# Performance work log

Measured on AMD Instinct MI355X. Metric: run time of the kernel, lower is better.

The kernel has to match this reference:

```python
import jax, jax.numpy as jnp
import numpy as np

BS, SEQ, DIM, DIM_MLP, E = 2, 2048, 1024, 4096, 8
STD = 0.02  # nn.init.normal_(weight, std=0.02)


def setup_inputs() -> dict:
    key = jax.random.key(0)
    k_x, k_idx, k_w1, k_w2 = jax.random.split(key, 4)
    x = jax.random.normal(k_x, (BS, SEQ, DIM), dtype=jnp.float32)
    expert_idx = jax.random.randint(k_idx, (BS, SEQ), 0, E, dtype=jnp.int32)
    W1 = jax.random.normal(k_w1, (E, DIM, DIM_MLP), dtype=jnp.float32) * STD
    b1 = jnp.zeros((E, DIM_MLP), dtype=jnp.float32)
    W2 = jax.random.normal(k_w2, (E, DIM_MLP, DIM), dtype=jnp.float32) * STD
    b2 = jnp.zeros((E, DIM), dtype=jnp.float32)
    return {"x": x, "expert_idx": expert_idx, "W1": W1, "b1": b1, "W2": W2, "b2": b2}


def reference(x, expert_idx, W1, b1, W2, b2):
    # Compute ALL experts on all tokens (faithful to the torch module).
    # h: [bs, seq, E, dim_mlp]
    h = jnp.einsum("bsd,edm->bsem", x, W1) + b1
    h = jax.nn.gelu(h, approximate=False)  # torch nn.GELU default = exact erf
    # feat: [bs, seq, E, dim]  (== torch.cat along feature dim, reshaped)
    feat = jnp.einsum("bsem,emd->bsed", h, W2) + b2
    # Per-token gather of the assigned expert's output (top-1 select).
    idx = expert_idx.astype(jnp.int32)[:, :, None, None]  # [bs, seq, 1, 1]
    out = jnp.take_along_axis(feat, idx, axis=2)[:, :, 0, :]  # [bs, seq, dim]
    return out
```

## Files before the change

### kernel.cpp

```cpp
#include <hip/hip_runtime.h>
#include <hip/hip_bf16.h>
#include <math.h>

#define TOK   4096
#define DIM   1024
#define DMLP  4096
#define NE    8
#define BM    128
#define BN    128
#define BN2   64
#define BK    64
#define PADMAX (TOK + NE * BM)
#define NTILES (PADMAX / BM)

typedef __attribute__((ext_vector_type(8))) short  short8;
typedef __attribute__((ext_vector_type(4))) float  float4v;
typedef __attribute__((ext_vector_type(4))) unsigned short ushort4v;

#define ASYNC16(gp, lp) __builtin_amdgcn_global_load_lds( \
    (const __attribute__((address_space(1))) unsigned int*)(gp), \
    (__attribute__((address_space(3))) unsigned int*)(lp), 16, 0, 0)

#define FRAG_OFF(R, C) (((((R) << 3) + ((C) ^ ((R) & 7)))) << 3)

static __device__ __forceinline__ unsigned short f2bf(float f) {
  unsigned u = __float_as_uint(f);
  u += 0x7fffu + ((u >> 16) & 1u);
  return (unsigned short)(u >> 16);
}

__global__ void group_kernel(const int* __restrict__ eidx,
                             int* __restrict__ perm,
                             int* __restrict__ tile_e) {
  __shared__ int cnt[NE], off[NE], len[NE], cur[NE];
  const int tid = threadIdx.x;
  if (tid < NE) cnt[tid] = 0;
  __syncthreads();
  for (int i = tid; i < TOK; i += 256) atomicAdd(&cnt[eidx[i]], 1);
  __syncthreads();
  if (tid == 0) {
    int o = 0;
    for (int e = 0; e < NE; e++) {
      off[e] = o;
      len[e] = ((cnt[e] + BM - 1) / BM) * BM;
      cur[e] = o;
      o += len[e];
    }
  }
  __syncthreads();
  for (int s = tid; s < PADMAX; s += 256) perm[s] = -1;
  __syncthreads();
  for (int i = tid; i < TOK; i += 256) {
    const int e = eidx[i];
    const int p = atomicAdd(&cur[e], 1);
    perm[p] = i;
  }
  __syncthreads();
  for (int t = tid; t < NTILES; t += 256) {
    const int row = t * BM;
    int te = -1;
    for (int e = 0; e < NE; e++)
      if (row >= off[e] && row < off[e] + len[e]) te = e;
    tile_e[t] = te;
  }
}

__global__ __launch_bounds__(256)
void convtrans_kernel(const float* __restrict__ W, unsigned short* __restrict__ WT,
                      int K, int N) {
  __shared__ unsigned short T[64][66];
  const int e  = blockIdx.z;
  const int k0 = blockIdx.y * 64, n0 = blockIdx.x * 64;
  const float* Win = W + (size_t)e * K * N;
  unsigned short* Wout = WT + (size_t)e * K * N;
  const int tid = threadIdx.x;
  const int nl  = tid & 63;
  const int kb  = (tid >> 6) * 16;
#pragma unroll
  for (int r = 0; r < 16; r++) {
    const int kl = kb + r;
    T[nl][kl] = f2bf(Win[(size_t)(k0 + kl) * N + n0 + nl]);
  }
  __syncthreads();
  const int kc = (tid & 31) * 2;
  const int nb = tid >> 5;
#pragma unroll
  for (int r = 0; r < 8; r++) {
    const int nl2 = nb + r * 8;
    const unsigned v = *(const unsigned*)&T[nl2][kc];
    *(unsigned*)&Wout[(size_t)(n0 + nl2) * K + k0 + kc] = v;
  }
}

__global__ __launch_bounds__(256)
void xgather_kernel(const float* __restrict__ x, const int* __restrict__ perm,
                    unsigned short* __restrict__ xg) {
  const int slot = blockIdx.x;
  const int t    = perm[slot];
  const int tid  = threadIdx.x;
  ushort4v o = (ushort4v){0, 0, 0, 0};
  if (t >= 0) {
    const float4v v = *(const float4v*)(x + (size_t)t * DIM + tid * 4);
#pragma unroll
    for (int q = 0; q < 4; q++) o[q] = f2bf(v[q]);
  }
  *(ushort4v*)(xg + (size_t)slot * DIM + tid * 4) = o;
}

__global__ __launch_bounds__(256)
void gemm1_kernel(const unsigned short* __restrict__ xg,
                  const unsigned short* __restrict__ W1T,
                  const float* __restrict__ b1, const int* __restrict__ tile_e,
                  unsigned short* __restrict__ h) {
  const int te = tile_e[blockIdx.x];
  if (te < 0) return;
  const unsigned short* Asrc = xg + (size_t)blockIdx.x * BM * DIM;
  const unsigned short* Bsrc = W1T + (size_t)te * DIM * DMLP + (size_t)(blockIdx.y * BN) * DIM;
  const int tid = threadIdx.x;

  __shared__ __align__(16) unsigned short As[BM * BK];
  __shared__ __align__(16) unsigned short Bs[BN * BK];

  const unsigned short* ag[4];
  const unsigned short* bg[4];
  int lo[4];
#pragma unroll
  for (int t = 0; t < 4; t++) {
    const int p = t * 256 + tid;
    const int r = p >> 3;
    const int c = (p & 7) ^ (r & 7);
    ag[t] = Asrc + (size_t)r * DIM + c * 8;
    bg[t] = Bsrc + (size_t)r * DIM + c * 8;
    lo[t] = p * 8;
  }

  const int wid = tid >> 6, lane = tid & 63;
  const int wm = (wid >> 1) * 64, wn = (wid & 1) * 64;
  const int l15 = lane & 15, quad = lane >> 4;

  float4v acc[4][4];
#pragma unroll
  for (int i = 0; i < 4; i++)
#pragma unroll
    for (int j = 0; j < 4; j++) acc[i][j] = (float4v){0.f, 0.f, 0.f, 0.f};

  for (int k0 = 0; k0 < DIM; k0 += BK) {
#pragma unroll
    for (int t = 0; t < 4; t++) ASYNC16(ag[t] + k0, &As[lo[t]]);
#pragma unroll
    for (int t = 0; t < 4; t++) ASYNC16(bg[t] + k0, &Bs[lo[t]]);
    __syncthreads();

#pragma unroll
    for (int hh = 0; hh < 2; hh++) {
      short8 a[4], b[4];
      const int C = hh * 4 + quad;
#pragma unroll
      for (int i = 0; i < 4; i++) a[i] = *(const short8*)&As[FRAG_OFF(wm + i * 16 + l15, C)];
#pragma unroll
      for (int j = 0; j < 4; j++) b[j] = *(const short8*)&Bs[FRAG_OFF(wn + j * 16 + l15, C)];
#pragma unroll
      for (int i = 0; i < 4; i++)
#pragma unroll
        for (int j = 0; j < 4; j++)
          acc[i][j] = __builtin_amdgcn_mfma_f32_16x16x32_bf16(a[i], b[j], acc[i][j], 0, 0, 0);
    }
    __syncthreads();
  }

#pragma unroll
  for (int i = 0; i < 4; i++) {
#pragma unroll
    for (int j = 0; j < 4; j++) {
      const int col = blockIdx.y * BN + wn + j * 16 + l15;
      const float bias = b1[te * DMLP + col];
#pragma unroll
      for (int r = 0; r < 4; r++) {
        const int row = wm + i * 16 + quad * 4 + r;
        float v = acc[i][j][r] + bias;
        v = 0.5f * v * (1.0f + erff(v * 0.7071067811865475f));
        h[(size_t)(blockIdx.x * BM + row) * DMLP + col] = f2bf(v);
      }
    }
  }
}

__global__ __launch_bounds__(256)
void gemm2_kernel(const unsigned short* __restrict__ h,
                  const unsigned short* __restrict__ W2T,
                  const float* __restrict__ b2, const int* __restrict__ perm,
                  const int* __restrict__ tile_e, float* __restrict__ out) {
  const int te = tile_e[blockIdx.x];
  if (te < 0) return;
  const unsigned short* Asrc = h + (size_t)blockIdx.x * BM * DMLP;
  const unsigned short* Bsrc = W2T + (size_t)te * DMLP * DIM + (size_t)(blockIdx.y * BN2) * DMLP;
  const int tid = threadIdx.x;

  __shared__ __align__(16) unsigned short As[BM * BK];
  __shared__ __align__(16) unsigned short Bs[BN2 * BK];

  const unsigned short* ag[4];
  const unsigned short* bg[2];
  int alo[4], blo[2];
#pragma unroll
  for (int t = 0; t < 4; t++) {
    const int p = t * 256 + tid;
    const int r = p >> 3;
    const int c = (p & 7) ^ (r & 7);
    ag[t] = Asrc + (size_t)r * DMLP + c * 8;
    alo[t] = p * 8;
  }
#pragma unroll
  for (int t = 0; t < 2; t++) {
    const int p = t * 256 + tid;
    const int r = p >> 3;
    const int c = (p & 7) ^ (r & 7);
    bg[t] = Bsrc + (size_t)r * DMLP + c * 8;
    blo[t] = p * 8;
  }

  const int wid = tid >> 6, lane = tid & 63;
  const int wm = (wid >> 1) * 64, wn = (wid & 1) * 32;
  const int l15 = lane & 15, quad = lane >> 4;

  float4v acc[4][2];
#pragma unroll
  for (int i = 0; i < 4; i++)
#pragma unroll
    for (int j = 0; j < 2; j++) acc[i][j] = (float4v){0.f, 0.f, 0.f, 0.f};

  for (int k0 = 0; k0 < DMLP; k0 += BK) {
#pragma unroll
    for (int t = 0; t < 4; t++) ASYNC16(ag[t] + k0, &As[alo[t]]);
#pragma unroll
    for (int t = 0; t < 2; t++) ASYNC16(bg[t] + k0, &Bs[blo[t]]);
    __syncthreads();

#pragma unroll
    for (int hh = 0; hh < 2; hh++) {
      short8 a[4], b[2];
      const int C = hh * 4 + quad;
#pragma unroll
      for (int i = 0; i < 4; i++) a[i] = *(const short8*)&As[FRAG_OFF(wm + i * 16 + l15, C)];
#pragma unroll
      for (int j = 0; j < 2; j++) b[j] = *(const short8*)&Bs[FRAG_OFF(wn + j * 16 + l15, C)];
#pragma unroll
      for (int i = 0; i < 4; i++)
#pragma unroll
        for (int j = 0; j < 2; j++)
          acc[i][j] = __builtin_amdgcn_mfma_f32_16x16x32_bf16(a[i], b[j], acc[i][j], 0, 0, 0);
    }
    __syncthreads();
  }

#pragma unroll
  for (int i = 0; i < 4; i++) {
#pragma unroll
    for (int j = 0; j < 2; j++) {
      const int col = blockIdx.y * BN2 + wn + j * 16 + l15;
      const float bias = b2[te * DIM + col];
#pragma unroll
      for (int r = 0; r < 4; r++) {
        const int row  = wm + i * 16 + quad * 4 + r;
        const int slot = blockIdx.x * BM + row;
        const int t    = perm[slot];
        if (t >= 0) out[(size_t)t * DIM + col] = acc[i][j][r] + bias;
      }
    }
  }
}

extern "C" void kernel_launch(void* const* d_in, const int* in_sizes, int n_in,
                              void* d_out, int out_size, void* d_ws, size_t ws_size,
                              hipStream_t stream) {
  const float* x    = (const float*)d_in[0];
  const int*   eidx = (const int*)d_in[1];
  const float* W1   = (const float*)d_in[2];
  const float* b1   = (const float*)d_in[3];
  const float* W2   = (const float*)d_in[4];
  const float* b2   = (const float*)d_in[5];
  float* out = (float*)d_out;

  char* ws = (char*)d_ws;
  int* perm   = (int*)ws;
  int* tile_e = (int*)(ws + PADMAX * sizeof(int));
  unsigned short* xg  = (unsigned short*)(ws + 32768);
  unsigned short* h   = (unsigned short*)(ws + 32768 + 10485760);
  unsigned short* W1T = (unsigned short*)(ws + 32768 + 10485760 + 41943040);
  unsigned short* W2T = (unsigned short*)((char*)W1T + 67108864);

  group_kernel<<<1, 256, 0, stream>>>(eidx, perm, tile_e);
  convtrans_kernel<<<dim3(DMLP / 64, DIM / 64, NE), 256, 0, stream>>>(W1, W1T, DIM, DMLP);
  convtrans_kernel<<<dim3(DIM / 64, DMLP / 64, NE), 256, 0, stream>>>(W2, W2T, DMLP, DIM);
  xgather_kernel<<<PADMAX, 256, 0, stream>>>(x, perm, xg);
  gemm1_kernel<<<dim3(NTILES, DMLP / BN), 256, 0, stream>>>(xg, W1T, b1, tile_e, h);
  gemm2_kernel<<<dim3(NTILES, DIM / BN2), 256, 0, stream>>>(h, W2T, b2, perm, tile_e, out);
}
```

Before: 494.3 us.

## Enlarge GEMM tiles to 256 rows, split-K GEMM2 with atomics, vectorize transpose, fast GELU

The row tile grows to 256 with 512-thread blocks in both GEMMs, and GEMM2 widens its N tile to 128 while splitting K four ways, accumulating into a zeroed output with float atomics. The weight convert-transpose kernel now uses vectorized float4 loads and 16-byte stores. The exact erff GELU is replaced by a polynomial erf approximation using rcp and exp. These changes target redundant weight traffic, occupancy, and epilogue cost, but larger tiles add more padding waste per expert. They also bring atomic contention, an extra zeroing pass, and a small accuracy change in GELU.

Measured after the change: 519.3 us. +5.0%, slower.

```diff
diff --git a/kernel.cpp b/kernel.cpp
--- a/kernel.cpp
+++ b/kernel.cpp
@@ -6,12 +6,14 @@
 #define DIM   1024
 #define DMLP  4096
 #define NE    8
-#define BM    128
+#define BM    256
 #define BN    128
-#define BN2   64
 #define BK    64
+#define NTHR  512
 #define PADMAX (TOK + NE * BM)
 #define NTILES (PADMAX / BM)
+#define KSPLIT 4
+#define KCHUNK (DMLP / KSPLIT)
 
 typedef __attribute__((ext_vector_type(8))) short  short8;
 typedef __attribute__((ext_vector_type(4))) float  float4v;
@@ -27,6 +29,22 @@
   unsigned u = __float_as_uint(f);
   u += 0x7fffu + ((u >> 16) & 1u);
   return (unsigned short)(u >> 16);
+}
+
+static __device__ __forceinline__ float gelu_f(float v) {
+  const float s = v * 0.7071067811865475f;
+  const float a = fabsf(s);
+  const float t = __builtin_amdgcn_rcpf(1.0f + 0.3275911f * a);
+  float p = 1.061405429f;
+  p = p * t - 1.453152027f;
+  p = p * t + 1.421413741f;
+  p = p * t - 0.284496736f;
+  p = p * t + 0.254829592f;
+  p = p * t;
+  const float e = __expf(-s * s);
+  float er = 1.0f - p * e;
+  er = copysignf(er, s);
+  return 0.5f * v * (1.0f + er);
 }
 
 __global__ void group_kernel(const int* __restrict__ eidx,
@@ -66,29 +84,43 @@
 }
 
 __global__ __launch_bounds__(256)
+void zero_out_kernel(float* __restrict__ out) {
+  const int i = blockIdx.x * 256 + threadIdx.x;
+  *(float4v*)(out + (size_t)i * 4) = (float4v){0.f, 0.f, 0.f, 0.f};
+}
+
+__global__ __launch_bounds__(256)
 void convtrans_kernel(const float* __restrict__ W, unsigned short* __restrict__ WT,
                       int K, int N) {
-  __shared__ unsigned short T[64][66];
+  __shared__ unsigned short T[64][68];
   const int e  = blockIdx.z;
   const int k0 = blockIdx.y * 64, n0 = blockIdx.x * 64;
   const float* Win = W + (size_t)e * K * N;
   unsigned short* Wout = WT + (size_t)e * K * N;
   const int tid = threadIdx.x;
-  const int nl  = tid & 63;
-  const int kb  = (tid >> 6) * 16;
-#pragma unroll
-  for (int r = 0; r < 16; r++) {
-    const int kl = kb + r;
-    T[nl][kl] = f2bf(Win[(size_t)(k0 + kl) * N + n0 + nl]);
-  }
-  __syncthreads();
-  const int kc = (tid & 31) * 2;
-  const int nb = tid >> 5;
-#pragma unroll
-  for (int r = 0; r < 8; r++) {
-    const int nl2 = nb + r * 8;
-    const unsigned v = *(const unsigned*)&T[nl2][kc];
-    *(unsigned*)&Wout[(size_t)(n0 + nl2) * K + k0 + kc] = v;
+
+  const int klb = tid >> 4;
+  const int n4  = (tid & 15) * 4;
+#pragma unroll
+  for (int r = 0; r < 4; r++) {
+    const int kl = klb + r * 16;
+    const float4v v = *(const float4v*)(Win + (size_t)(k0 + kl) * N + n0 + n4);
+#pragma unroll
+    for (int q = 0; q < 4; q++) T[n4 + q][kl] = f2bf(v[q]);
+  }
+  __syncthreads();
+
+  const int nlb = tid >> 3;
+  const int kc  = (tid & 7) * 8;
+#pragma unroll
+  for (int w = 0; w < 2; w++) {
+    const int nl = nlb + w * 32;
+    const ushort4v u0 = *(const ushort4v*)&T[nl][kc];
+    const ushort4v u1 = *(const ushort4v*)&T[nl][kc + 4];
+    short8 o;
+#pragma unroll
+    for (int q = 0; q < 4; q++) { o[q] = (short)u0[q]; o[q + 4] = (short)u1[q]; }
+    *(short8*)(Wout + (size_t)(n0 + nl) * K + k0 + kc) = o;
   }
 }
 
@@ -107,7 +139,7 @@
   *(ushort4v*)(xg + (size_t)slot * DIM + tid * 4) = o;
 }
 
-__global__ __launch_bounds__(256)
+__global__ __launch_bounds__(NTHR)
 void gemm1_kernel(const unsigned short* __restrict__ xg,
                   const unsigned short* __restrict__ W1T,
                   const float* __restrict__ b1, const int* __restrict__ tile_e,
@@ -122,16 +154,23 @@
   __shared__ __align__(16) unsigned short Bs[BN * BK];
 
   const unsigned short* ag[4];
-  const unsigned short* bg[4];
-  int lo[4];
+  const unsigned short* bg[2];
+  int alo[4], blo[2];
 #pragma unroll
   for (int t = 0; t < 4; t++) {
-    const int p = t * 256 + tid;
+    const int p = t * NTHR + tid;
     const int r = p >> 3;
     const int c = (p & 7) ^ (r & 7);
     ag[t] = Asrc + (size_t)r * DIM + c * 8;
+    alo[t] = p * 8;
+  }
+#pragma unroll
+  for (int t = 0; t < 2; t++) {
+    const int p = t * NTHR + tid;
+    const int r = p >> 3;
+    const int c = (p & 7) ^ (r & 7);
     bg[t] = Bsrc + (size_t)r * DIM + c * 8;
-    lo[t] = p * 8;
+    blo[t] = p * 8;
   }
 
   const int wid = tid >> 6, lane = tid & 63;
@@ -146,9 +185,9 @@
 
   for (int k0 = 0; k0 < DIM; k0 += BK) {
 #pragma unroll
-    for (int t = 0; t < 4; t++) ASYNC16(ag[t] + k0, &As[lo[t]]);
-#pragma unroll
-    for (int t = 0; t < 4; t++) ASYNC16(bg[t] + k0, &Bs[lo[t]]);
+    for (int t = 0; t < 4; t++) ASYNC16(ag[t] + k0, &As[alo[t]]);
+#pragma unroll
+    for (int t = 0; t < 2; t++) ASYNC16(bg[t] + k0, &Bs[blo[t]]);
     __syncthreads();
 
 #pragma unroll
@@ -177,34 +216,35 @@
 #pragma unroll
       for (int r = 0; r < 4; r++) {
         const int row = wm + i * 16 + quad * 4 + r;
-        float v = acc[i][j][r] + bias;
-        v = 0.5f * v * (1.0f + erff(v * 0.7071067811865475f));
+        const float v = gelu_f(acc[i][j][r] + bias);
         h[(size_t)(blockIdx.x * BM + row) * DMLP + col] = f2bf(v);
       }
     }
   }
 }
 
-__global__ __launch_bounds__(256)
+__global__ __launch_bounds__(NTHR)
 void gemm2_kernel(const unsigned short* __restrict__ h,
                   const unsigned short* __restrict__ W2T,
                   const float* __restrict__ b2, const int* __restrict__ perm,
                   const int* __restrict__ tile_e, float* __restrict__ out) {
   const int te = tile_e[blockIdx.x];
   if (te < 0) return;
-  const unsigned short* Asrc = h + (size_t)blockIdx.x * BM * DMLP;
-  const unsigned short* Bsrc = W2T + (size_t)te * DMLP * DIM + (size_t)(blockIdx.y * BN2) * DMLP;
+  const int kbase = blockIdx.z * KCHUNK;
+  const unsigned short* Asrc = h + (size_t)blockIdx.x * BM * DMLP + kbase;
+  const unsigned short* Bsrc = W2T + (size_t)te * DMLP * DIM
+                             + (size_t)(blockIdx.y * BN) * DMLP + kbase;
   const int tid = threadIdx.x;
 
   __shared__ __align__(16) unsigned short As[BM * BK];
-  __shared__ __align__(16) unsigned short Bs[BN2 * BK];
+  __shared__ __align__(16) unsigned short Bs[BN * BK];
 
   const unsigned short* ag[4];
   const unsigned short* bg[2];
   int alo[4], blo[2];
 #pragma unroll
   for (int t = 0; t < 4; t++) {
-    const int p = t * 256 + tid;
+    const int p = t * NTHR + tid;
     const int r = p >> 3;
     const int c = (p & 7) ^ (r & 7);
     ag[t] = Asrc + (size_t)r * DMLP + c * 8;
@@ -212,7 +252,7 @@
   }
 #pragma unroll
   for (int t = 0; t < 2; t++) {
-    const int p = t * 256 + tid;
+    const int p = t * NTHR + tid;
     const int r = p >> 3;
     const int c = (p & 7) ^ (r & 7);
     bg[t] = Bsrc + (size_t)r * DMLP + c * 8;
@@ -220,16 +260,16 @@
   }
 
   const int wid = tid >> 6, lane = tid & 63;
-  const int wm = (wid >> 1) * 64, wn = (wid & 1) * 32;
+  const int wm = (wid >> 1) * 64, wn = (wid & 1) * 64;
   const int l15 = lane & 15, quad = lane >> 4;
 
-  float4v acc[4][2];
+  float4v acc[4][4];
 #pragma unroll
   for (int i = 0; i < 4; i++)
 #pragma unroll
-    for (int j = 0; j < 2; j++) acc[i][j] = (float4v){0.f, 0.f, 0.f, 0.f};
-
-  for (int k0 = 0; k0 < DMLP; k0 += BK) {
+    for (int j = 0; j < 4; j++) acc[i][j] = (float4v){0.f, 0.f, 0.f, 0.f};
+
+  for (int k0 = 0; k0 < KCHUNK; k0 += BK) {
 #pragma unroll
     for (int t = 0; t < 4; t++) ASYNC16(ag[t] + k0, &As[alo[t]]);
 #pragma unroll
@@ -238,16 +278,16 @@
 
 #pragma unroll
     for (int hh = 0; hh < 2; hh++) {
-      short8 a[4], b[2];
+      short8 a[4], b[4];
       const int C = hh * 4 + quad;
 #pragma unroll
       for (int i = 0; i < 4; i++) a[i] = *(const short8*)&As[FRAG_OFF(wm + i * 16 + l15, C)];
 #pragma unroll
-      for (int j = 0; j < 2; j++) b[j] = *(const short8*)&Bs[FRAG_OFF(wn + j * 16 + l15, C)];
+      for (int j = 0; j < 4; j++) b[j] = *(const short8*)&Bs[FRAG_OFF(wn + j * 16 + l15, C)];
 #pragma unroll
       for (int i = 0; i < 4; i++)
 #pragma unroll
-        for (int j = 0; j < 2; j++)
+        for (int j = 0; j < 4; j++)
           acc[i][j] = __builtin_amdgcn_mfma_f32_16x16x32_bf16(a[i], b[j], acc[i][j], 0, 0, 0);
     }
     __syncthreads();
@@ -256,15 +296,15 @@
 #pragma unroll
   for (int i = 0; i < 4; i++) {
 #pragma unroll
-    for (int j = 0; j < 2; j++) {
-      const int col = blockIdx.y * BN2 + wn + j * 16 + l15;
-      const float bias = b2[te * DIM + col];
+    for (int j = 0; j < 4; j++) {
+      const int col = blockIdx.y * BN + wn + j * 16 + l15;
+      const float bias = (blockIdx.z == 0) ? b2[te * DIM + col] : 0.f;
 #pragma unroll
       for (int r = 0; r < 4; r++) {
         const int row  = wm + i * 16 + quad * 4 + r;
         const int slot = blockIdx.x * BM + row;
         const int t    = perm[slot];
-        if (t >= 0) out[(size_t)t * DIM + col] = acc[i][j][r] + bias;
+        if (t >= 0) atomicAdd(&out[(size_t)t * DIM + col], acc[i][j][r] + bias);
       }
     }
   }
@@ -285,14 +325,15 @@
   int* perm   = (int*)ws;
   int* tile_e = (int*)(ws + PADMAX * sizeof(int));
   unsigned short* xg  = (unsigned short*)(ws + 32768);
-  unsigned short* h   = (unsigned short*)(ws + 32768 + 10485760);
-  unsigned short* W1T = (unsigned short*)(ws + 32768 + 10485760 + 41943040);
-  unsigned short* W2T = (unsigned short*)((char*)W1T + 67108864);
+  unsigned short* h   = (unsigned short*)((char*)xg + (size_t)PADMAX * DIM * 2);
+  unsigned short* W1T = (unsigned short*)((char*)h + (size_t)PADMAX * DMLP * 2);
+  unsigned short* W2T = (unsigned short*)((char*)W1T + (size_t)NE * DIM * DMLP * 2);
 
   group_kernel<<<1, 256, 0, stream>>>(eidx, perm, tile_e);
+  zero_out_kernel<<<(TOK * DIM) / 1024, 256, 0, stream>>>(out);
   convtrans_kernel<<<dim3(DMLP / 64, DIM / 64, NE), 256, 0, stream>>>(W1, W1T, DIM, DMLP);
   convtrans_kernel<<<dim3(DIM / 64, DMLP / 64, NE), 256, 0, stream>>>(W2, W2T, DMLP, DIM);
   xgather_kernel<<<PADMAX, 256, 0, stream>>>(x, perm, xg);
-  gemm1_kernel<<<dim3(NTILES, DMLP / BN), 256, 0, stream>>>(xg, W1T, b1, tile_e, h);
-  gemm2_kernel<<<dim3(NTILES, DIM / BN2), 256, 0, stream>>>(h, W2T, b2, perm, tile_e, out);
-}
+  gemm1_kernel<<<dim3(NTILES, DMLP / BN), NTHR, 0, stream>>>(xg, W1T, b1, tile_e, h);
+  gemm2_kernel<<<dim3(NTILES, DIM / BN, KSPLIT), NTHR, 0, stream>>>(h, W2T, b2, perm, tile_e, out);
+}
```
